# Performance work log

Measured on AMD Instinct MI355X. Metric: run time of the kernel, lower is better.

The kernel has to match this reference:

```python
import jax, jax.numpy as jnp
import numpy as np

N_LINEARS = 16
CHANNELS = 3
OUTPUT_DIM = 64
Z_DIM = 128
BATCH = 512


def hash_vectors(z, n):
    # Deterministic surrogate for repo's hash_vectors: map each latent vector
    # to an integer bucket in [0, n). Data-dependent, jit-compatible.
    s = jnp.abs(jnp.sum(z, axis=1)) * 1000.0
    return jnp.mod(jnp.floor(s).astype(jnp.int32), n)


def setup_inputs() -> dict:
    key = jax.random.key(0)
    k1, k2, k3 = jax.random.split(key, 3)
    out_features = CHANNELS * OUTPUT_DIM ** 2 * N_LINEARS  # 196608
    z = jax.random.normal(k1, (BATCH, Z_DIM), dtype=jnp.float32)
    # Linear weight stored as (out_features, in_features), torch convention.
    W = jax.random.normal(k2, (out_features, Z_DIM), dtype=jnp.float32) * (1.0 / np.sqrt(Z_DIM))
    b = jax.random.normal(k3, (out_features,), dtype=jnp.float32) * 0.01
    return {"z": z, "W": W, "b": b}


def reference(z, W, b):
    B = z.shape[0]
    # Dense GEMM: (B, out_features)
    out = jnp.einsum('bi,oi->bo', z, W) + b
    out = out.reshape(B, N_LINEARS, CHANNELS, OUTPUT_DIM, OUTPUT_DIM)
    c = hash_vectors(z, N_LINEARS)  # (B,) int32 in [0, N_LINEARS)
    # Per-sample gather of one linear's output block.
    return jnp.take_along_axis(out, c[:, None, None, None, None], axis=1)[:, 0]
```

## Files before the change

### kernel.cpp

```cpp
#include <hip/hip_runtime.h>
#include <hip/hip_bf16.h>
#include <math.h>


#define N_LINEARS 16
#define ZD 128
#define BATCH 512
#define BLOCK_OUT 12288
#define STILE 48
#define SLOTS 64
#define ZROWS (ZD + 1)
#define TJ 256

typedef float vf16 __attribute__((ext_vector_type(16)));
typedef vf16 vf16u __attribute__((aligned(16)));

#define LISTS_OFF 16
#define BP_OFF (36864 / 4)
#define ZG_OFF_BYTES 65536

__global__ __launch_bounds__(512) void hash_kernel(
    const float* __restrict__ z, int* __restrict__ counts,
    int* __restrict__ lists, int* __restrict__ bp) {
  __shared__ int cnt[N_LINEARS];
  const int b = threadIdx.x;
  if (b < N_LINEARS) cnt[b] = 0;
  __syncthreads();

  const float4* zr4 = (const float4*)(z + b * ZD);
  const float4 pa = zr4[0], pb = zr4[1];
  float r0 = pa.x, r1 = pa.y, r2 = pa.z, r3 = pa.w;
  float r4 = pb.x, r5 = pb.y, r6 = pb.z, r7 = pb.w;
  #pragma unroll
  for (int i = 2; i < ZD / 4; i += 2) {
    const float4 a = zr4[i], d = zr4[i + 1];
    r0 += a.x; r1 += a.y; r2 += a.z; r3 += a.w;
    r4 += d.x; r5 += d.y; r6 += d.z; r7 += d.w;
  }
  float res = ((r0 + r1) + (r2 + r3)) + ((r4 + r5) + (r6 + r7));
  float v = fabsf(res) * 1000.0f;
  int cb = ((int)floorf(v)) & (N_LINEARS - 1);

  int pos = atomicAdd(&cnt[cb], 1);
  lists[(cb << 9) + pos] = b;
  bp[b] = cb | (pos << 4);

  __syncthreads();
  if (b < N_LINEARS) counts[b] = cnt[b];
}

__global__ __launch_bounds__(128) void gather_kernel(
    const float* __restrict__ z, const int* __restrict__ bp,
    float* __restrict__ zgT) {
  const int b = blockIdx.x;
  const int k = threadIdx.x;
  const int v = bp[b];
  const int cb = v & 15;
  const int pos = v >> 4;
  if (pos < SLOTS)
    zgT[(size_t)cb * (ZROWS * SLOTS) + (size_t)k * SLOTS + pos] = z[b * ZD + k];
}


#define ZL(N0, N1, N2, K1)                                           \
  { const vf16u* zr_ = (const vf16u*)(zp + (K1) * SLOTS);            \
    N0 = zr_[0];                                                     \
    if constexpr (NV >= 2) N1 = zr_[1];                              \
    if constexpr (NV >= 3) N2 = zr_[2]; }

#define ZF(C0, C1, C2, WK)                                           \
  { const float wk_ = (WK);                                          \
    vf16 wv_;                                                        \
    _Pragma("unroll") for (int e = 0; e < 16; ++e) wv_[e] = wk_;     \
    acc0 += C0 * wv_;                                                \
    if constexpr (NV >= 2) acc1 += C1 * wv_;                         \
    if constexpr (NV >= 3) acc2 += C2 * wv_; }

#define STEP(C0, C1, C2, N0, N1, N2, K1, WK)                         \
  ZL(N0, N1, N2, K1) ZF(C0, C1, C2, WK)

template <int NV>
__device__ __forceinline__ void tile_body(
    const float* __restrict__ zp,
    const float4* __restrict__ Wv, float bj,
    float* __restrict__ out, const int* lst, int m, int j) {
  vf16 acc0, acc1, acc2;
  _Pragma("unroll") for (int e = 0; e < 16; ++e) acc0[e] = bj;
  if constexpr (NV >= 2) {
    _Pragma("unroll") for (int e = 0; e < 16; ++e) acc1[e] = bj;
  }
  if constexpr (NV >= 3) {
    _Pragma("unroll") for (int e = 0; e < 16; ++e) acc2[e] = bj;
  }

  vf16 zA0, zA1, zA2, zB0, zB1, zB2;
  ZL(zA0, zA1, zA2, 0)
  float4 wq  = Wv[0];
  float4 wqn = Wv[1];

  for (int kc = 0; kc < ZD / 4; ++kc) {
    const int k0 = kc * 4;
    STEP(zA0, zA1, zA2, zB0, zB1, zB2, k0 + 1, wq.x)
    STEP(zB0, zB1, zB2, zA0, zA1, zA2, k0 + 2, wq.y)
    STEP(zA0, zA1, zA2, zB0, zB1, zB2, k0 + 3, wq.z)
    STEP(zB0, zB1, zB2, zA0, zA1, zA2, k0 + 4, wq.w)
    wq = wqn;
    const int wi = kc + 2 > 31 ? 31 : kc + 2;
    wqn = Wv[wi];
  }

  _Pragma("unroll") for (int t = 0; t < 16; ++t)
    if (t < m) out[(size_t)lst[t] * BLOCK_OUT + j] = acc0[t];
  if constexpr (NV >= 2) {
    _Pragma("unroll") for (int t = 0; t < 16; ++t)
      if (16 + t < m) out[(size_t)lst[16 + t] * BLOCK_OUT + j] = acc1[t];
  }
  if constexpr (NV >= 3) {
    _Pragma("unroll") for (int t = 0; t < 16; ++t)
      if (32 + t < m) out[(size_t)lst[32 + t] * BLOCK_OUT + j] = acc2[t];
  }
}

__global__ __launch_bounds__(TJ, 3) void gen_main_kernel(
    const float* __restrict__ W, const float* __restrict__ bias,
    float* __restrict__ out, const int* __restrict__ counts,
    const int* __restrict__ lists, const float* __restrict__ zgT) {
  __shared__ float zsh[ZROWS * SLOTS];
  __shared__ int   lsh[SLOTS];
  const int c = blockIdx.y;
  const int j = blockIdx.x * TJ + threadIdx.x;
  int n = counts[c];
  n = n > SLOTS ? SLOTS : n;
  if (n == 0) return;

  {
    const float4* zg4 = (const float4*)(zgT + (size_t)c * (ZROWS * SLOTS));
    float4* ls4 = (float4*)zsh;
    #pragma unroll
    for (int i = 0; i < 9; ++i) {
      const int idx = threadIdx.x + i * TJ;
      if (idx < (ZROWS * SLOTS) / 4) ls4[idx] = zg4[idx];
    }
    if (threadIdx.x < SLOTS) lsh[threadIdx.x] = lists[(c << 9) + threadIdx.x];
  }
  __syncthreads();

  const size_t row = (size_t)c * BLOCK_OUT + (size_t)j;
  const float4* __restrict__ Wv = (const float4*)(W + row * (size_t)ZD);
  const float bj = bias[row];

  for (int s0 = 0; s0 < n; s0 += STILE) {
    const int mm = n - s0;
    const int m = mm > STILE ? STILE : mm;
    if (m <= 16)
      tile_body<1>(zsh + s0, Wv, bj, out, lsh + s0, m, j);
    else if (m <= 32)
      tile_body<2>(zsh + s0, Wv, bj, out, lsh + s0, m, j);
    else
      tile_body<3>(zsh + s0, Wv, bj, out, lsh + s0, m, j);
  }
}

extern "C" void kernel_launch(void* const* d_in, const int* in_sizes, int n_in,
                              void* d_out, int out_size, void* d_ws, size_t ws_size,
                              hipStream_t stream) {
  const float* z    = (const float*)d_in[0];
  const float* W    = (const float*)d_in[1];
  const float* bias = (const float*)d_in[2];
  float* out = (float*)d_out;

  int*   counts = (int*)d_ws;
  int*   lists  = (int*)d_ws + LISTS_OFF;
  int*   bp     = (int*)d_ws + BP_OFF;
  float* zgT    = (float*)((char*)d_ws + ZG_OFF_BYTES);

  hipLaunchKernelGGL(hash_kernel, dim3(1), dim3(BATCH), 0, stream,
                     z, counts, lists, bp);
  hipLaunchKernelGGL(gather_kernel, dim3(BATCH), dim3(ZD), 0, stream,
                     z, bp, zgT);

  dim3 grid(BLOCK_OUT / TJ, N_LINEARS);
  hipLaunchKernelGGL(gen_main_kernel, grid, dim3(TJ), 0, stream,
                     W, bias, out, counts, lists, zgT);
}
```

Before: 206.1 us.

## Shrink shared z tile to 48 slots and use vf4 accumulators with wider W prefetch

The per-bucket z tile in shared memory now holds only 48 sample slots instead of 64. Samples beyond 48 are handled by reloading the tile with the remaining columns after a barrier and running a second pass. The inner loop switches from 16-wide vector register blocks to arrays of 4-wide vectors, reading z from LDS per k with broadcast weights, and prefetches 16 W values at a time instead of 4. This is meant to cut LDS footprint and register pressure to raise occupancy, at the cost of more LDS reads and an extra barrier-and-reload path for large buckets.

```diff
diff --git a/kernel.cpp b/kernel.cpp
--- a/kernel.cpp
+++ b/kernel.cpp
@@ -11,9 +11,9 @@
 #define SLOTS 64
 #define ZROWS (ZD + 1)
 #define TJ 256
+#define SS 48
 
-typedef float vf16 __attribute__((ext_vector_type(16)));
-typedef vf16 vf16u __attribute__((aligned(16)));
+typedef float vf4 __attribute__((ext_vector_type(4)));
 
 #define LISTS_OFF 16
 #define BP_OFF (36864 / 4)
@@ -62,70 +62,55 @@
 }
 
 
-#define ZL(N0, N1, N2, K1)                                           \
-  { const vf16u* zr_ = (const vf16u*)(zp + (K1) * SLOTS);            \
-    N0 = zr_[0];                                                     \
-    if constexpr (NV >= 2) N1 = zr_[1];                              \
-    if constexpr (NV >= 3) N2 = zr_[2]; }
-
-#define ZF(C0, C1, C2, WK)                                           \
-  { const float wk_ = (WK);                                          \
-    vf16 wv_;                                                        \
-    _Pragma("unroll") for (int e = 0; e < 16; ++e) wv_[e] = wk_;     \
-    acc0 += C0 * wv_;                                                \
-    if constexpr (NV >= 2) acc1 += C1 * wv_;                         \
-    if constexpr (NV >= 3) acc2 += C2 * wv_; }
-
-#define STEP(C0, C1, C2, N0, N1, N2, K1, WK)                         \
-  ZL(N0, N1, N2, K1) ZF(C0, C1, C2, WK)
-
 template <int NV>
 __device__ __forceinline__ void tile_body(
-    const float* __restrict__ zp,
-    const float4* __restrict__ Wv, float bj,
-    float* __restrict__ out, const int* lst, int m, int j) {
-  vf16 acc0, acc1, acc2;
-  _Pragma("unroll") for (int e = 0; e < 16; ++e) acc0[e] = bj;
-  if constexpr (NV >= 2) {
-    _Pragma("unroll") for (int e = 0; e < 16; ++e) acc1[e] = bj;
-  }
-  if constexpr (NV >= 3) {
-    _Pragma("unroll") for (int e = 0; e < 16; ++e) acc2[e] = bj;
+    const float* __restrict__ zs,
+    const vf4* __restrict__ Wv, float bj,
+    float* __restrict__ out, const int* __restrict__ lst, int m, int j) {
+  vf4 acc[NV * 4];
+  #pragma unroll
+  for (int q = 0; q < NV * 4; ++q) acc[q] = (vf4){bj, bj, bj, bj};
+
+  vf4 wc[4], wn[4];
+  #pragma unroll
+  for (int i = 0; i < 4; ++i) wc[i] = Wv[i];
+
+  for (int c8 = 0; c8 < 8; ++c8) {
+    const int base = (c8 + 1) * 4;
+    #pragma unroll
+    for (int i = 0; i < 4; ++i) {
+      int wi = base + i;
+      wi = wi > 31 ? 31 : wi;
+      wn[i] = Wv[wi];
+    }
+    #pragma unroll
+    for (int q4 = 0; q4 < 4; ++q4) {
+      #pragma unroll
+      for (int e = 0; e < 4; ++e) {
+        const int k = c8 * 16 + q4 * 4 + e;
+        const float wk = wc[q4][e];
+        const vf4 wv = {wk, wk, wk, wk};
+        #pragma unroll
+        for (int q = 0; q < NV * 4; ++q) {
+          const vf4 zq = *(const vf4*)&zs[k * SS + q * 4];
+          acc[q] += zq * wv;
+        }
+      }
+    }
+    #pragma unroll
+    for (int i = 0; i < 4; ++i) wc[i] = wn[i];
   }
 
-  vf16 zA0, zA1, zA2, zB0, zB1, zB2;
-  ZL(zA0, zA1, zA2, 0)
-  float4 wq  = Wv[0];
-  float4 wqn = Wv[1];
-
-  for (int kc = 0; kc < ZD / 4; ++kc) {
-    const int k0 = kc * 4;
-    STEP(zA0, zA1, zA2, zB0, zB1, zB2, k0 + 1, wq.x)
-    STEP(zB0, zB1, zB2, zA0, zA1, zA2, k0 + 2, wq.y)
-    STEP(zA0, zA1, zA2, zB0, zB1, zB2, k0 + 3, wq.z)
-    STEP(zB0, zB1, zB2, zA0, zA1, zA2, k0 + 4, wq.w)
-    wq = wqn;
-    const int wi = kc + 2 > 31 ? 31 : kc + 2;
-    wqn = Wv[wi];
-  }
-
-  _Pragma("unroll") for (int t = 0; t < 16; ++t)
-    if (t < m) out[(size_t)lst[t] * BLOCK_OUT + j] = acc0[t];
-  if constexpr (NV >= 2) {
-    _Pragma("unroll") for (int t = 0; t < 16; ++t)
-      if (16 + t < m) out[(size_t)lst[16 + t] * BLOCK_OUT + j] = acc1[t];
-  }
-  if constexpr (NV >= 3) {
-    _Pragma("unroll") for (int t = 0; t < 16; ++t)
-      if (32 + t < m) out[(size_t)lst[32 + t] * BLOCK_OUT + j] = acc2[t];
-  }
+  #pragma unroll
+  for (int t = 0; t < NV * 16; ++t)
+    if (t < m) out[(size_t)lst[t] * BLOCK_OUT + j] = acc[t >> 2][t & 3];
 }
 
 __global__ __launch_bounds__(TJ, 3) void gen_main_kernel(
     const float* __restrict__ W, const float* __restrict__ bias,
     float* __restrict__ out, const int* __restrict__ counts,
     const int* __restrict__ lists, const float* __restrict__ zgT) {
-  __shared__ float zsh[ZROWS * SLOTS];
+  __shared__ float zsh[ZROWS * SS];
   __shared__ int   lsh[SLOTS];
   const int c = blockIdx.y;
   const int j = blockIdx.x * TJ + threadIdx.x;
@@ -133,31 +118,40 @@
   n = n > SLOTS ? SLOTS : n;
   if (n == 0) return;
 
+  const float* __restrict__ zg = zgT + (size_t)c * (ZROWS * SLOTS);
   {
-    const float4* zg4 = (const float4*)(zgT + (size_t)c * (ZROWS * SLOTS));
-    float4* ls4 = (float4*)zsh;
     #pragma unroll
-    for (int i = 0; i < 9; ++i) {
+    for (int i = 0; i < 6; ++i) {
       const int idx = threadIdx.x + i * TJ;
-      if (idx < (ZROWS * SLOTS) / 4) ls4[idx] = zg4[idx];
+      const int k = idx / 12, q = idx % 12;
+      *(vf4*)&zsh[k * SS + q * 4] = *(const vf4*)&zg[k * SLOTS + q * 4];
     }
     if (threadIdx.x < SLOTS) lsh[threadIdx.x] = lists[(c << 9) + threadIdx.x];
   }
   __syncthreads();
 
   const size_t row = (size_t)c * BLOCK_OUT + (size_t)j;
-  const float4* __restrict__ Wv = (const float4*)(W + row * (size_t)ZD);
+  const vf4* __restrict__ Wv = (const vf4*)(W + row * (size_t)ZD);
   const float bj = bias[row];
 
-  for (int s0 = 0; s0 < n; s0 += STILE) {
-    const int mm = n - s0;
-    const int m = mm > STILE ? STILE : mm;
-    if (m <= 16)
-      tile_body<1>(zsh + s0, Wv, bj, out, lsh + s0, m, j);
-    else if (m <= 32)
-      tile_body<2>(zsh + s0, Wv, bj, out, lsh + s0, m, j);
-    else
-      tile_body<3>(zsh + s0, Wv, bj, out, lsh + s0, m, j);
+  const int m1 = n > STILE ? STILE : n;
+  if (m1 <= 16)
+    tile_body<1>(zsh, Wv, bj, out, lsh, m1, j);
+  else if (m1 <= 32)
+    tile_body<2>(zsh, Wv, bj, out, lsh, m1, j);
+  else
+    tile_body<3>(zsh, Wv, bj, out, lsh, m1, j);
+
+  if (n > STILE) {
+    __syncthreads();
+    #pragma unroll
+    for (int i = 0; i < 2; ++i) {
+      const int idx = threadIdx.x + i * TJ;
+      const int k = idx >> 2, q = idx & 3;
+      *(vf4*)&zsh[k * SS + q * 4] = *(const vf4*)&zg[k * SLOTS + STILE + q * 4];
+    }
+    __syncthreads();
+    tile_body<1>(zsh, Wv, bj, out, lsh + STILE, n - STILE, j);
   }
 }
 
```

Measured after the change: 208.6 us. About the same (+1.2%).
